# Kernel optimization log

Hardware: AMD Instinct MI355X
Metric: run time of the kernel (lower is better)

Reference implementation:

```python
import jax, jax.numpy as jnp
import numpy as np


def setup_inputs() -> dict:
    key = jax.random.key(0)
    k1, k2, k3, k4 = jax.random.split(key, 4)
    B, C, H, W = 16, 64, 128, 128
    x = jax.random.normal(k1, (B, C, H, W), dtype=jnp.float32)
    y = jax.random.normal(k2, (B, C, H, W), dtype=jnp.float32)
    # nn.Parameter(torch.zeros(1)) in the original; use small random values so
    # the attention branch contributes (zeros would make it a pure residual).
    temperature1 = jax.random.normal(k3, (1,), dtype=jnp.float32) * 0.1
    temperature2 = jax.random.normal(k4, (1,), dtype=jnp.float32) * 0.1
    return {"x": x, "y": y, "temperature1": temperature1,
            "temperature2": temperature2, "num_heads": 4}


def _l2norm_lastdim(v):
    # F.normalize(v, dim=-1): v / max(||v||_2, eps)
    n = jnp.sqrt(jnp.sum(v * v, axis=-1, keepdims=True))
    return v / jnp.maximum(n, 1e-12)


def reference(x, y, temperature1, temperature2, num_heads):
    B, C, H, W = x.shape
    c = C // num_heads
    HW = H * W
    # b (head c) h w -> b head c (h w)
    xr = x.reshape(B, num_heads, c, HW)
    yr = y.reshape(B, num_heads, c, HW)

    # key_x normalized over (h w); key_y (b head (hw) c) normalized over dim=-2,
    # which is the same (h w) axis of yr in 'bhck' layout.
    key_x = _l2norm_lastdim(xr)
    key_y = _l2norm_lastdim(yr)
    # energy[b,h,c,d] = sum_k key_x[b,h,c,k] * key_y[b,h,d,k]  -> (B, head, c, c)
    energy = jnp.einsum('bhck,bhdk->bhcd', key_x, key_y)

    attn1 = jax.nn.softmax(energy, axis=-1)                        # (B,h,c,c)
    attn2 = jax.nn.softmax(energy.transpose(0, 1, 3, 2), axis=-1)  # (B,h,c,c)

    # y_att (b head (hw) c) = value_y @ attn1, then 'b head (h w) c -> b (head c) h w'
    # out[b,h,d,k] = sum_c attn1[b,h,c,d] * yr[b,h,c,k]
    y_att = jnp.einsum('bhcd,bhck->bhdk', attn1, yr).reshape(B, C, H, W)
    x_att = jnp.einsum('bhcd,bhck->bhdk', attn2, xr).reshape(B, C, H, W)

    y_ = temperature1[0] * y_att + x
    x_ = temperature2[0] * x_att + y
    return jnp.concatenate((x_, y_), axis=1)  # (B, 2C, H, W)
```

## Files before the change

kernel.cpp:

```cpp
#include <hip/hip_runtime.h>

#define HW    16384
#define CPH   16
#define NBH   64
#define KSLICE 2048
#define TKT   256
#define LS    260
#define KPT   4

#define WS_SX   16384
#define WS_SY   17408
#define WS_W    18432
#define WS_ZERO_BYTES (18432 * 4)

__global__ __launch_bounds__(256) void gram_kernel(
    const float* __restrict__ x,
    const float* __restrict__ y,
    float* __restrict__ ws)
{
    __shared__ float xs[16 * LS];
    __shared__ float ys[16 * LS];
    __shared__ float Gs[256];
    __shared__ float sxs[16], sys[16];

    const int blk = blockIdx.x;
    const int bh  = blk >> 3;
    const int ks  = (blk & 7) * KSLICE;
    const int t   = threadIdx.x;

    Gs[t] = 0.f;
    if (t < 16) { sxs[t] = 0.f; sys[t] = 0.f; }

    const int c0 = t & 3;
    const int d0 = (t >> 2) & 3;
    const int g  = t >> 4;

    float acc[4][4];
    #pragma unroll
    for (int i = 0; i < 4; ++i)
        #pragma unroll
        for (int j = 0; j < 4; ++j) acc[i][j] = 0.f;
    float sqx[4] = {0.f, 0.f, 0.f, 0.f};
    float sqy[4] = {0.f, 0.f, 0.f, 0.f};

    const float* xb = x + (size_t)bh * CPH * HW + ks;
    const float* yb = y + (size_t)bh * CPH * HW + ks;

    for (int kt = 0; kt < KSLICE; kt += TKT) {
        __syncthreads();
        #pragma unroll
        for (int i = 0; i < 4; ++i) {
            int idx = i * 256 + t;
            int row = idx >> 6;
            int col = (idx & 63) * 4;
            float4 xv = *reinterpret_cast<const float4*>(xb + (size_t)row * HW + kt + col);
            float4 yv = *reinterpret_cast<const float4*>(yb + (size_t)row * HW + kt + col);
            *reinterpret_cast<float4*>(&xs[row * LS + col]) = xv;
            *reinterpret_cast<float4*>(&ys[row * LS + col]) = yv;
        }
        __syncthreads();

        #pragma unroll
        for (int kq = 0; kq < 16; kq += 4) {
            float4 xr[4], yr[4];
            #pragma unroll
            for (int i = 0; i < 4; ++i)
                xr[i] = *reinterpret_cast<const float4*>(&xs[(c0 + 4 * i) * LS + g * 16 + kq]);
            #pragma unroll
            for (int j = 0; j < 4; ++j)
                yr[j] = *reinterpret_cast<const float4*>(&ys[(d0 + 4 * j) * LS + g * 16 + kq]);
            #pragma unroll
            for (int i = 0; i < 4; ++i)
                #pragma unroll
                for (int j = 0; j < 4; ++j) {
                    acc[i][j] = fmaf(xr[i].x, yr[j].x, acc[i][j]);
                    acc[i][j] = fmaf(xr[i].y, yr[j].y, acc[i][j]);
                    acc[i][j] = fmaf(xr[i].z, yr[j].z, acc[i][j]);
                    acc[i][j] = fmaf(xr[i].w, yr[j].w, acc[i][j]);
                }
            if (d0 == 0) {
                #pragma unroll
                for (int i = 0; i < 4; ++i) {
                    sqx[i] = fmaf(xr[i].x, xr[i].x, sqx[i]);
                    sqx[i] = fmaf(xr[i].y, xr[i].y, sqx[i]);
                    sqx[i] = fmaf(xr[i].z, xr[i].z, sqx[i]);
                    sqx[i] = fmaf(xr[i].w, xr[i].w, sqx[i]);
                }
            }
            if (c0 == 0) {
                #pragma unroll
                for (int j = 0; j < 4; ++j) {
                    sqy[j] = fmaf(yr[j].x, yr[j].x, sqy[j]);
                    sqy[j] = fmaf(yr[j].y, yr[j].y, sqy[j]);
                    sqy[j] = fmaf(yr[j].z, yr[j].z, sqy[j]);
                    sqy[j] = fmaf(yr[j].w, yr[j].w, sqy[j]);
                }
            }
        }
    }

    #pragma unroll
    for (int i = 0; i < 4; ++i)
        #pragma unroll
        for (int j = 0; j < 4; ++j)
            atomicAdd(&Gs[(c0 + 4 * i) * 16 + (d0 + 4 * j)], acc[i][j]);
    if (d0 == 0) {
        #pragma unroll
        for (int i = 0; i < 4; ++i) atomicAdd(&sxs[c0 + 4 * i], sqx[i]);
    }
    if (c0 == 0) {
        #pragma unroll
        for (int j = 0; j < 4; ++j) atomicAdd(&sys[d0 + 4 * j], sqy[j]);
    }
    __syncthreads();
    atomicAdd(&ws[bh * 256 + t], Gs[t]);
    if (t < 16)       atomicAdd(&ws[WS_SX + bh * 16 + t], sxs[t]);
    else if (t < 32)  atomicAdd(&ws[WS_SY + bh * 16 + (t - 16)], sys[t - 16]);
}

__global__ __launch_bounds__(256) void softmax_kernel(
    float* __restrict__ ws,
    const float* __restrict__ t1p,
    const float* __restrict__ t2p)
{
    const int bh = blockIdx.x;
    const int t  = threadIdx.x;
    const int i  = t >> 4;
    const int j  = t & 15;

    __shared__ float Es[256];

    float nx = fmaxf(sqrtf(ws[WS_SX + bh * 16 + i]), 1e-12f);
    float ny = fmaxf(sqrtf(ws[WS_SY + bh * 16 + j]), 1e-12f);
    float e  = ws[bh * 256 + i * 16 + j] / (nx * ny);
    Es[t] = e;
    __syncthreads();

    float rm = -1e30f;
    #pragma unroll
    for (int r = 0; r < 16; ++r) rm = fmaxf(rm, Es[i * 16 + r]);
    float rs = 0.f;
    #pragma unroll
    for (int r = 0; r < 16; ++r) rs += expf(Es[i * 16 + r] - rm);
    float a1 = expf(e - rm) / rs;

    float cm = -1e30f;
    #pragma unroll
    for (int r = 0; r < 16; ++r) cm = fmaxf(cm, Es[r * 16 + j]);
    float cs = 0.f;
    #pragma unroll
    for (int r = 0; r < 16; ++r) cs += expf(Es[r * 16 + j] - cm);
    float v2 = expf(e - cm) / cs;

    const float t1 = t1p[0];
    const float t2 = t2p[0];

    float* W = ws + WS_W + bh * 512;
    W[(i * 16 + j) * 2 + 1] = t1 * a1;
    W[(j * 16 + i) * 2 + 0] = t2 * v2;
}

__global__ __launch_bounds__(256) void apply_kernel(
    const float* __restrict__ x,
    const float* __restrict__ y,
    const float* __restrict__ ws,
    float* __restrict__ out)
{
    const int CHUNKS = HW / (256 * KPT);
    const int blk   = blockIdx.x;
    const int bh    = blk / CHUNKS;
    const int chunk = blk % CHUNKS;
    const int t     = threadIdx.x;
    const int k0    = chunk * (256 * KPT) + t * KPT;

    __shared__ float2 Ws[256];
    Ws[t] = reinterpret_cast<const float2*>(ws + WS_W)[bh * 256 + t];
    __syncthreads();

    const int b = bh >> 2;
    const int h = bh & 3;

    const float* xbase = x + ((size_t)bh * CPH) * HW + k0;
    const float* ybase = y + ((size_t)bh * CPH) * HW + k0;

    float accx[16][KPT];
    float accy[16][KPT];
    #pragma unroll
    for (int d = 0; d < 16; ++d)
        #pragma unroll
        for (int j = 0; j < KPT; ++j) { accx[d][j] = 0.f; accy[d][j] = 0.f; }

    float4 xq = *reinterpret_cast<const float4*>(xbase);
    float4 yq = *reinterpret_cast<const float4*>(ybase);
    #pragma unroll
    for (int c = 0; c < 16; ++c) {
        float4 xn, yn;
        if (c < 15) {
            xn = *reinterpret_cast<const float4*>(xbase + (size_t)(c + 1) * HW);
            yn = *reinterpret_cast<const float4*>(ybase + (size_t)(c + 1) * HW);
        }
        float xv[KPT] = {xq.x, xq.y, xq.z, xq.w};
        float yv[KPT] = {yq.x, yq.y, yq.z, yq.w};
        #pragma unroll
        for (int d = 0; d < 16; ++d) {
            float2 w = Ws[c * 16 + d];
            #pragma unroll
            for (int j = 0; j < KPT; ++j) accx[d][j] = fmaf(w.x, xv[j], accx[d][j]);
            #pragma unroll
            for (int j = 0; j < KPT; ++j) accy[d][j] = fmaf(w.y, yv[j], accy[d][j]);
        }
        #pragma unroll
        for (int j = 0; j < KPT; ++j) accx[c][j] += yv[j];
        #pragma unroll
        for (int j = 0; j < KPT; ++j) accy[c][j] += xv[j];
        xq = xn; yq = yn;
    }

    const size_t obx = ((size_t)b * 128 + h * 16) * HW + k0;
    const size_t oby = obx + (size_t)64 * HW;
    #pragma unroll
    for (int d = 0; d < 16; ++d) {
        float4 px = make_float4(accx[d][0], accx[d][1], accx[d][2], accx[d][3]);
        float4 py = make_float4(accy[d][0], accy[d][1], accy[d][2], accy[d][3]);
        *reinterpret_cast<float4*>(out + obx + (size_t)d * HW) = px;
        *reinterpret_cast<float4*>(out + oby + (size_t)d * HW) = py;
    }
}

extern "C" void kernel_launch(void* const* d_in, const int* in_sizes, int n_in,
                              void* d_out, int out_size, void* d_ws, size_t ws_size,
                              hipStream_t stream) {
    const float* x  = (const float*)d_in[0];
    const float* y  = (const float*)d_in[1];
    const float* t1 = (const float*)d_in[2];
    const float* t2 = (const float*)d_in[3];
    float* ws  = (float*)d_ws;
    float* out = (float*)d_out;

    hipMemsetAsync(d_ws, 0, WS_ZERO_BYTES, stream);
    gram_kernel<<<NBH * 8, 256, 0, stream>>>(x, y, ws);
    softmax_kernel<<<NBH, 256, 0, stream>>>(ws, t1, t2);
    apply_kernel<<<NBH * (HW / (256 * KPT)), 256, 0, stream>>>(x, y, ws, out);
}
```

Measured before the change: 277.3 us.

## Drop memset and softmax kernel; write per-slice partials and fuse softmax into apply

The gram kernel now writes per-slice partial Gram matrices and squared norms to distinct workspace slots instead of using global atomics. This removes the workspace memset, and the slice count doubles to 16 for more blocks. The softmax kernel is removed: each apply block reduces the 16 partials for its head, then computes both softmaxes and the temperature-scaled weights in shared memory. This cuts two launches and the global atomics, at the cost of every apply block repeating the small reduction and softmax.

```diff
diff --git a/kernel.cpp b/kernel.cpp
--- a/kernel.cpp
+++ b/kernel.cpp
@@ -1,17 +1,15 @@
 #include <hip/hip_runtime.h>
 
-#define HW    16384
-#define CPH   16
-#define NBH   64
-#define KSLICE 2048
-#define TKT   256
-#define LS    260
-#define KPT   4
-
-#define WS_SX   16384
-#define WS_SY   17408
-#define WS_W    18432
-#define WS_ZERO_BYTES (18432 * 4)
+#define HW      16384
+#define CPH     16
+#define NBH     64
+#define NSLICE  16
+#define KSLICE  (HW / NSLICE)
+#define TKT     256
+#define LS      260
+#define KPT     4
+#define PSTRIDE 288
+
 
 __global__ __launch_bounds__(256) void gram_kernel(
     const float* __restrict__ x,
@@ -24,8 +22,9 @@
     __shared__ float sxs[16], sys[16];
 
     const int blk = blockIdx.x;
-    const int bh  = blk >> 3;
-    const int ks  = (blk & 7) * KSLICE;
+    const int bh  = blk >> 4;
+    const int sl  = blk & 15;
+    const int ks  = sl * KSLICE;
     const int t   = threadIdx.x;
 
     Gs[t] = 0.f;
@@ -113,57 +112,19 @@
         for (int j = 0; j < 4; ++j) atomicAdd(&sys[d0 + 4 * j], sqy[j]);
     }
     __syncthreads();
-    atomicAdd(&ws[bh * 256 + t], Gs[t]);
-    if (t < 16)       atomicAdd(&ws[WS_SX + bh * 16 + t], sxs[t]);
-    else if (t < 32)  atomicAdd(&ws[WS_SY + bh * 16 + (t - 16)], sys[t - 16]);
-}
-
-__global__ __launch_bounds__(256) void softmax_kernel(
-    float* __restrict__ ws,
-    const float* __restrict__ t1p,
-    const float* __restrict__ t2p)
-{
-    const int bh = blockIdx.x;
-    const int t  = threadIdx.x;
-    const int i  = t >> 4;
-    const int j  = t & 15;
-
-    __shared__ float Es[256];
-
-    float nx = fmaxf(sqrtf(ws[WS_SX + bh * 16 + i]), 1e-12f);
-    float ny = fmaxf(sqrtf(ws[WS_SY + bh * 16 + j]), 1e-12f);
-    float e  = ws[bh * 256 + i * 16 + j] / (nx * ny);
-    Es[t] = e;
-    __syncthreads();
-
-    float rm = -1e30f;
-    #pragma unroll
-    for (int r = 0; r < 16; ++r) rm = fmaxf(rm, Es[i * 16 + r]);
-    float rs = 0.f;
-    #pragma unroll
-    for (int r = 0; r < 16; ++r) rs += expf(Es[i * 16 + r] - rm);
-    float a1 = expf(e - rm) / rs;
-
-    float cm = -1e30f;
-    #pragma unroll
-    for (int r = 0; r < 16; ++r) cm = fmaxf(cm, Es[r * 16 + j]);
-    float cs = 0.f;
-    #pragma unroll
-    for (int r = 0; r < 16; ++r) cs += expf(Es[r * 16 + j] - cm);
-    float v2 = expf(e - cm) / cs;
-
-    const float t1 = t1p[0];
-    const float t2 = t2p[0];
-
-    float* W = ws + WS_W + bh * 512;
-    W[(i * 16 + j) * 2 + 1] = t1 * a1;
-    W[(j * 16 + i) * 2 + 0] = t2 * v2;
+
+    float* P = ws + (size_t)(bh * NSLICE + sl) * PSTRIDE;
+    P[t] = Gs[t];
+    if (t < 16)       P[256 + t] = sxs[t];
+    else if (t < 32)  P[272 + (t - 16)] = sys[t - 16];
 }
 
 __global__ __launch_bounds__(256) void apply_kernel(
     const float* __restrict__ x,
     const float* __restrict__ y,
     const float* __restrict__ ws,
+    const float* __restrict__ t1p,
+    const float* __restrict__ t2p,
     float* __restrict__ out)
 {
     const int CHUNKS = HW / (256 * KPT);
@@ -172,9 +133,52 @@
     const int chunk = blk % CHUNKS;
     const int t     = threadIdx.x;
     const int k0    = chunk * (256 * KPT) + t * KPT;
-
+    const int i     = t >> 4;
+    const int j     = t & 15;
+
+    __shared__ float  Es[256];
     __shared__ float2 Ws[256];
-    Ws[t] = reinterpret_cast<const float2*>(ws + WS_W)[bh * 256 + t];
+    __shared__ float  nxs[16], nys[16];
+
+    const float* P = ws + (size_t)bh * NSLICE * PSTRIDE;
+    float gsum = 0.f;
+    #pragma unroll
+    for (int s = 0; s < NSLICE; ++s) gsum += P[s * PSTRIDE + t];
+    if (t < 32) {
+        const int off = (t < 16) ? (256 + t) : (272 + (t - 16));
+        float q = 0.f;
+        #pragma unroll
+        for (int s = 0; s < NSLICE; ++s) q += P[s * PSTRIDE + off];
+        float n = fmaxf(sqrtf(q), 1e-12f);
+        if (t < 16) nxs[t] = n; else nys[t - 16] = n;
+    }
+    __syncthreads();
+
+    const float e = gsum / (nxs[i] * nys[j]);
+    Es[t] = e;
+    __syncthreads();
+
+    float rm = -1e30f;
+    #pragma unroll
+    for (int r = 0; r < 16; ++r) rm = fmaxf(rm, Es[i * 16 + r]);
+    float rs = 0.f;
+    #pragma unroll
+    for (int r = 0; r < 16; ++r) rs += expf(Es[i * 16 + r] - rm);
+    const float a1 = expf(e - rm) / rs;
+
+    float cm = -1e30f;
+    #pragma unroll
+    for (int r = 0; r < 16; ++r) cm = fmaxf(cm, Es[r * 16 + j]);
+    float cs = 0.f;
+    #pragma unroll
+    for (int r = 0; r < 16; ++r) cs += expf(Es[r * 16 + j] - cm);
+    const float v2 = expf(e - cm) / cs;
+
+    const float t1 = t1p[0];
+    const float t2 = t2p[0];
+    float* Wsf = reinterpret_cast<float*>(Ws);
+    Wsf[(i * 16 + j) * 2 + 1] = t1 * a1;
+    Wsf[(j * 16 + i) * 2 + 0] = t2 * v2;
     __syncthreads();
 
     const int b = bh >> 2;
@@ -188,7 +192,7 @@
     #pragma unroll
     for (int d = 0; d < 16; ++d)
         #pragma unroll
-        for (int j = 0; j < KPT; ++j) { accx[d][j] = 0.f; accy[d][j] = 0.f; }
+        for (int q = 0; q < KPT; ++q) { accx[d][q] = 0.f; accy[d][q] = 0.f; }
 
     float4 xq = *reinterpret_cast<const float4*>(xbase);
     float4 yq = *reinterpret_cast<const float4*>(ybase);
@@ -205,14 +209,14 @@
         for (int d = 0; d < 16; ++d) {
             float2 w = Ws[c * 16 + d];
             #pragma unroll
-            for (int j = 0; j < KPT; ++j) accx[d][j] = fmaf(w.x, xv[j], accx[d][j]);
-            #pragma unroll
-            for (int j = 0; j < KPT; ++j) accy[d][j] = fmaf(w.y, yv[j], accy[d][j]);
-        }
-        #pragma unroll
-        for (int j = 0; j < KPT; ++j) accx[c][j] += yv[j];
-        #pragma unroll
-        for (int j = 0; j < KPT; ++j) accy[c][j] += xv[j];
+            for (int q = 0; q < KPT; ++q) accx[d][q] = fmaf(w.x, xv[q], accx[d][q]);
+            #pragma unroll
+            for (int q = 0; q < KPT; ++q) accy[d][q] = fmaf(w.y, yv[q], accy[d][q]);
+        }
+        #pragma unroll
+        for (int q = 0; q < KPT; ++q) accx[c][q] += yv[q];
+        #pragma unroll
+        for (int q = 0; q < KPT; ++q) accy[c][q] += xv[q];
         xq = xn; yq = yn;
     }
 
@@ -237,8 +241,6 @@
     float* ws  = (float*)d_ws;
     float* out = (float*)d_out;
 
-    hipMemsetAsync(d_ws, 0, WS_ZERO_BYTES, stream);
-    gram_kernel<<<NBH * 8, 256, 0, stream>>>(x, y, ws);
-    softmax_kernel<<<NBH, 256, 0, stream>>>(ws, t1, t2);
-    apply_kernel<<<NBH * (HW / (256 * KPT)), 256, 0, stream>>>(x, y, ws, out);
+    gram_kernel<<<NBH * NSLICE, 256, 0, stream>>>(x, y, ws);
+    apply_kernel<<<NBH * (HW / (256 * KPT)), 256, 0, stream>>>(x, y, ws, t1, t2, out);
 }
```

Result: slower. 291.2 us (+5.0%).
